# Optimization experiments

Hardware: AMD Instinct MI355X
Metric: run time of the kernel (lower is better)

## Reference

```python
import jax, jax.numpy as jnp
import numpy as np
import math

B, S, D_MODEL = 2, 2048, 1024
H = 16
DK = D_MODEL // H          # 64, down-proj per-stream dim
NOPE, ROPE = 128, 64
D_HEAD = NOPE + ROPE       # 192 = d_latent // H
D_LATENT = H * D_HEAD      # 3072
ROT_DIM = 2 * ((ROPE // 2) // 2)  # rotary dim actually rotated = qk_rope_dim//2 = 32
EPS = 1e-6


def _rmsnorm(x, w):
    out = x * jax.lax.rsqrt(jnp.mean(x * x, axis=-1, keepdims=True) + EPS)
    return out * w


def _apply_rope(x):
    # x: [b, h, s, d]; rotate first ROT_DIM channels, interleaved pairing
    s = x.shape[-2]
    inv_freq = 1.0 / (10000.0 ** (jnp.arange(0, ROT_DIM, 2, dtype=jnp.float32) / ROT_DIM))
    freqs = jnp.arange(s, dtype=jnp.float32)[:, None] * inv_freq[None, :]  # [s, ROT_DIM//2]
    freqs = jnp.repeat(freqs, 2, axis=-1)  # [s, ROT_DIM], (f0,f0,f1,f1,...)
    cos, sin = jnp.cos(freqs), jnp.sin(freqs)
    xl, xr = x[..., :ROT_DIM], x[..., ROT_DIM:]
    x1, x2 = xl[..., 0::2], xl[..., 1::2]
    rot = jnp.stack([-x2, x1], axis=-1).reshape(xl.shape)
    xl = xl * cos + rot * sin
    return jnp.concatenate([xl, xr], axis=-1)


def setup_inputs() -> dict:
    key = jax.random.key(0)
    ks = jax.random.split(key, 5)
    sc = 0.02
    x = jax.random.normal(ks[0], (B, S, D_MODEL), jnp.float32)
    mask = jnp.broadcast_to(jnp.tril(jnp.ones((S, S), jnp.int32)), (B, S, S))
    w_down = jax.random.normal(ks[1], (D_MODEL, 3 * DK), jnp.float32) * sc
    rms_w = jnp.ones((3 * DK,), jnp.float32)
    w_up = jax.random.normal(ks[2], (3 * DK, 3 * D_LATENT), jnp.float32) * sc
    w_o = jax.random.normal(ks[3], (D_LATENT, D_MODEL), jnp.float32) * sc
    return {"x": x, "mask": mask, "w_down": w_down, "rms_w": rms_w, "w_up": w_up, "w_o": w_o}


def reference(x, mask, w_down, rms_w, w_up, w_o):
    h = x @ w_down                        # [b, s, 3*dk]
    h = _rmsnorm(h, rms_w)
    qkv = h @ w_up                        # [b, s, 3*d_latent]
    q, k, v = jnp.split(qkv, 3, axis=-1)  # each [b, s, d_latent]

    def to_heads(t):
        # einops '(d h)': d outer, h inner
        return t.reshape(B, S, D_HEAD, H).transpose(0, 3, 1, 2)  # [b, h, s, d]

    q, k, v = to_heads(q), to_heads(k), to_heads(v)
    q_nope, q_rope = q[..., :NOPE], q[..., NOPE:]
    k_nope, k_rope = k[..., :NOPE], k[..., NOPE:]
    q_rope = _apply_rope(q_rope)
    k_rope = _apply_rope(k_rope)

    scores = (jnp.einsum('bhid,bhjd->bhij', q_nope, k_nope)
              + jnp.einsum('bhid,bhjd->bhij', q_rope, k_rope))
    scores = scores / math.sqrt(NOPE + ROPE)
    scores = jnp.where(mask[:, None] == 0, -1e9, scores)
    attn = jax.nn.softmax(scores, axis=-1)

    out = jnp.einsum('bhij,bhjd->bhid', attn, v)        # [b, h, s, d]
    out = out.transpose(0, 2, 1, 3).reshape(B, S, D_LATENT)  # 'b h s d -> b s (h d)'
    return out @ w_o
```

## Files before the change

### kernel.cpp

```cpp
#include <hip/hip_runtime.h>
#include <stdint.h>
#include <stddef.h>


typedef __bf16 bf16x8 __attribute__((ext_vector_type(8)));
typedef float  f32x4  __attribute__((ext_vector_type(4)));

#define MFMA16x16(a,b,c) __builtin_amdgcn_mfma_f32_16x16x32_bf16((a),(b),(c),0,0,0)

__device__ __forceinline__ uint16_t f2bf(float f){
  union { float f; uint32_t u; } v; v.f = f;
  uint32_t u = v.u + 0x7fffu + ((v.u >> 16) & 1u);
  return (uint16_t)(u >> 16);
}
__device__ __forceinline__ bf16x8 load_frag(const uint16_t* p){
  uint4 u = *reinterpret_cast<const uint4*>(p);
  return __builtin_bit_cast(bf16x8, u);
}
__device__ __forceinline__ f32x4 fzero(){
  f32x4 z = {0.f, 0.f, 0.f, 0.f};
  return z;
}
__device__ __forceinline__ uint32_t pack2(float a, float b){
  return (uint32_t)f2bf(a) | ((uint32_t)f2bf(b) << 16);
}
__device__ __forceinline__ void gl2lds16(const uint16_t* g, uint16_t* l){
  __builtin_amdgcn_global_load_lds(
      (const __attribute__((address_space(1))) uint32_t*)g,
      (__attribute__((address_space(3))) uint32_t*)l,
      16, 0, 0);
}

__global__ __launch_bounds__(256) void k_transpose_cvt(const float* __restrict__ in,
                                                       uint16_t* __restrict__ out,
                                                       int R, int C){
  __shared__ float t[32][33];
  const int tc = blockIdx.x * 32;
  const int tr = blockIdx.y * 32;
  const int j = threadIdx.x & 31, i0 = threadIdx.x >> 5;
  for(int ii = 0; ii < 4; ++ii){
    int r = i0 + ii * 8;
    t[r][j] = in[(size_t)(tr + r) * C + tc + j];
  }
  __syncthreads();
  for(int ii = 0; ii < 4; ++ii){
    int c = i0 + ii * 8;
    out[(size_t)(tc + c) * R + tr + j] = f2bf(t[j][c]);
  }
}

__global__ __launch_bounds__(256) void k_down_mfma(const float* __restrict__ x,
                                                   const uint16_t* __restrict__ wdt,
                                                   const float* __restrict__ rms_w,
                                                   uint16_t* __restrict__ h_out){
  __shared__ __align__(16) uint16_t as[32 * 64];
  __shared__ float hsq[32];
  const int tid  = threadIdx.x;
  const int wave = tid >> 6, lane = tid & 63;
  const int ml = lane & 15, qd = lane >> 4;
  const int m0 = blockIdx.x * 32;
  const int n0w = wave * 48;
  if(tid < 32) hsq[tid] = 0.f;

  f32x4 acc[2][3];
#pragma unroll
  for(int mt = 0; mt < 2; ++mt)
#pragma unroll
    for(int nt = 0; nt < 3; ++nt) acc[mt][nt] = fzero();

  const int srow = tid >> 3, sc = tid & 7;
  for(int kt = 0; kt < 16; ++kt){
    const float* src = x + (size_t)(m0 + srow) * 1024 + kt * 64 + sc * 8;
    float4 a = *reinterpret_cast<const float4*>(src);
    float4 b = *reinterpret_cast<const float4*>(src + 4);
    uint4 pk;
    pk.x = pack2(a.x, a.y); pk.y = pack2(a.z, a.w);
    pk.z = pack2(b.x, b.y); pk.w = pack2(b.z, b.w);
    __syncthreads();
    *reinterpret_cast<uint4*>(as + srow * 64 + ((sc ^ (srow & 7)) * 8)) = pk;
    __syncthreads();
#pragma unroll
    for(int kk = 0; kk < 2; ++kk){
      bf16x8 af[2];
#pragma unroll
      for(int mt = 0; mt < 2; ++mt){
        int row = mt * 16 + ml;
        af[mt] = load_frag(as + row * 64 + (((kk * 4 + qd) ^ (row & 7)) * 8));
      }
#pragma unroll
      for(int nt = 0; nt < 3; ++nt){
        bf16x8 bfr = load_frag(wdt + (size_t)(n0w + nt * 16 + ml) * 1024 + kt * 64 + kk * 32 + qd * 8);
#pragma unroll
        for(int mt = 0; mt < 2; ++mt)
          acc[mt][nt] = MFMA16x16(af[mt], bfr, acc[mt][nt]);
      }
    }
  }
  __syncthreads();
#pragma unroll
  for(int mt = 0; mt < 2; ++mt)
#pragma unroll
    for(int r = 0; r < 4; ++r){
      float s = acc[mt][0][r]*acc[mt][0][r] + acc[mt][1][r]*acc[mt][1][r] + acc[mt][2][r]*acc[mt][2][r];
#pragma unroll
      for(int off = 1; off < 16; off <<= 1) s += __shfl_xor(s, off);
      if(ml == 0) atomicAdd(&hsq[mt * 16 + qd * 4 + r], s);
    }
  __syncthreads();
  float rw[3];
#pragma unroll
  for(int nt = 0; nt < 3; ++nt) rw[nt] = rms_w[n0w + nt * 16 + ml];
#pragma unroll
  for(int mt = 0; mt < 2; ++mt)
#pragma unroll
    for(int r = 0; r < 4; ++r){
      int row = mt * 16 + qd * 4 + r;
      float scl = rsqrtf(hsq[row] * (1.0f / 192.0f) + 1e-6f);
#pragma unroll
      for(int nt = 0; nt < 3; ++nt)
        h_out[(size_t)(m0 + row) * 192 + n0w + nt * 16 + ml] = f2bf(acc[mt][nt][r] * scl * rw[nt]);
    }
}

__global__ __launch_bounds__(256) void k_gemm_up(const uint16_t* __restrict__ hmat,
                                                 const uint16_t* __restrict__ wt,
                                                 uint16_t* __restrict__ q_t,
                                                 uint16_t* __restrict__ k_t,
                                                 uint16_t* __restrict__ v_t){
  __shared__ __align__(16) uint16_t rp[16 * 129 * 8];
  const int wave = threadIdx.x >> 6, lane = threadIdx.x & 63;
  const int ml = lane & 15, qd = lane >> 4;
  const int m0 = blockIdx.y * 32;
  const int bx = blockIdx.x;
  const int which = bx / 6;
  const int d0b = (bx % 6) * 32;
  const int n0w = bx * 512 + wave * 128;
  const int d0w = d0b + wave * 8;

  bf16x8 af[2][6];
#pragma unroll
  for(int mt = 0; mt < 2; ++mt)
#pragma unroll
    for(int kk = 0; kk < 6; ++kk)
      af[mt][kk] = load_frag(hmat + (size_t)(m0 + mt * 16 + ml) * 192 + kk * 32 + qd * 8);

  f32x4 acc[8][2];
#pragma unroll
  for(int nt = 0; nt < 8; ++nt){ acc[nt][0] = fzero(); acc[nt][1] = fzero(); }
#pragma unroll
  for(int nt = 0; nt < 8; ++nt){
#pragma unroll
    for(int kk = 0; kk < 6; ++kk){
      bf16x8 b = load_frag(wt + (size_t)(n0w + nt * 16 + ml) * 192 + kk * 32 + qd * 8);
      acc[nt][0] = MFMA16x16(af[0][kk], b, acc[nt][0]);
      acc[nt][1] = MFMA16x16(af[1][kk], b, acc[nt][1]);
    }
  }

  const int b   = m0 >> 11;
  const int s0  = m0 & 2047;
  const int kt2 = s0 >> 6;
  const int row0 = s0 & 63;
  uint4* rp4 = (uint4*)rp;

  if(which < 2){
    const float qs = which ? 1.0f : 0.07216878364870322f;
    const bool rope = (d0w >= 128) && (d0w < 160);
#pragma unroll
    for(int mt = 0; mt < 2; ++mt)
#pragma unroll
      for(int r = 0; r < 4; ++r){
        int t = mt * 16 + qd * 4 + r;
        int s = s0 + t;
        float v[8];
#pragma unroll
        for(int nt = 0; nt < 8; ++nt) v[nt] = acc[nt][mt][r] * qs;
        if(rope){
#pragma unroll
          for(int pi = 0; pi < 4; ++pi){
            int fi = (d0w + 2 * pi - 128) >> 1;
            float invf = __expf(-(float)fi * 0.5756462732485114f);
            float sn, cs;
            sincosf((float)s * invf, &sn, &cs);
            float e = v[2 * pi], o = v[2 * pi + 1];
            v[2 * pi]     = e * cs - o * sn;
            v[2 * pi + 1] = o * cs + e * sn;
          }
        }
        uint4 pk;
        pk.x = pack2(v[0], v[1]); pk.y = pack2(v[2], v[3]);
        pk.z = pack2(v[4], v[5]); pk.w = pack2(v[6], v[7]);
        rp4[ml * 129 + t * 4 + (wave ^ (t & 3))] = pk;
      }
  } else {
#pragma unroll
    for(int nt = 0; nt < 8; ++nt){
      int dl = wave * 8 + nt;
#pragma unroll
      for(int mt = 0; mt < 2; ++mt){
        int jc = mt * 2 + (qd >> 1);
        int slot = ml * 129 + dl * 4 + (jc ^ (dl & 3));
        uint2 pk;
        pk.x = pack2(acc[nt][mt][0], acc[nt][mt][1]);
        pk.y = pack2(acc[nt][mt][2], acc[nt][mt][3]);
        *(reinterpret_cast<uint2*>(rp + slot * 8) + (qd & 1)) = pk;
      }
    }
  }
  __syncthreads();

  if(which < 2){
    uint16_t* dst = which ? k_t : q_t;
    const int cb = d0b >> 3;
#pragma unroll
    for(int it = 0; it < 8; ++it){
      int h = wave * 4 + (it & 3), rhalf = it >> 2;
      int tloc = rhalf * 16 + (lane >> 2), p = lane & 3;
      int row = row0 + tloc;
      uint4 val = rp4[h * 129 + tloc * 4 + p];
      size_t off = ((size_t)(b * 16 + h) * 32 + kt2) * 12288
                 + (size_t)row * 192 + ((cb ^ (tloc & 4)) + p) * 8;
      *reinterpret_cast<uint4*>(dst + off) = val;
    }
  } else {
    const int cs0 = row0 >> 3;
#pragma unroll
    for(int it = 0; it < 8; ++it){
      int h = wave * 4 + (it & 3), dhalf = it >> 2;
      int dl = dhalf * 16 + (lane >> 2), p = lane & 3;
      uint4 val = rp4[h * 129 + dl * 4 + p];
      size_t off = ((size_t)(b * 16 + h) * 32 + kt2) * 12288
                 + (size_t)(d0b + dl) * 64 + ((cs0 ^ (dl & 4)) + p) * 8;
      *reinterpret_cast<uint4*>(v_t + off) = val;
    }
  }
}

__global__ __launch_bounds__(512, 4) void k_attn(const uint16_t* __restrict__ q_t,
                                                 const uint16_t* __restrict__ k_t,
                                                 const uint16_t* __restrict__ v_t,
                                                 uint16_t* __restrict__ attn_out){
  __shared__ __align__(16) uint16_t smem[30720];
  const int tid  = threadIdx.x;
  const int wave = tid >> 6;
  const int lane = tid & 63;
  const int ml   = lane & 15;
  const int qd   = lane >> 4;
  const int B    = blockIdx.x;
  const int bh   = B & 31;
  const int prr  = B >> 5;
  const int qb   = (prr < 8) ? (15 - prr) : (prr - 8);
  const int last = 4 * qb + 3;

  uint16_t* const kbuf0 = smem;
  uint16_t* const kbuf1 = smem + 6144;
  uint16_t* const vbuf0 = smem + 12288;
  uint16_t* const vbuf1 = smem + 18944;
  uint16_t* const psw   = smem + 25600 + wave * 640;

  const uint16_t* kbase = k_t + (size_t)bh * 393216;
  const uint16_t* vbase = v_t + (size_t)bh * 393216;
  const uint16_t* qbase = q_t + (size_t)bh * 393216 + (size_t)qb * 24576;
  const int hh = bh & 15, bb = bh >> 4;

  int voffE[3], voffO[3];
  {
    const int w3 = (wave & 3) * 3;
#pragma unroll
    for(int it = 0; it < 3; ++it){
      int seg = w3 + it;
      int rp_ = seg * 8 + (lane >> 3);
      int x   = (lane & 7) ^ (rp_ & 7);
      int d   = rp_ * 2 + (x >> 2);
      int c   = x & 3;
      voffE[it] = d * 64 + (((0 + c) ^ (d & 7)) * 8);
      voffO[it] = d * 64 + (((4 + c) ^ (d & 7)) * 8);
    }
  }
  const int vpoff = (ml >> 1) * 64 + ((((ml & 1) * 4 + qd) ^ (ml >> 1)) * 8);

  {
    const int s0 = wave * 6;
#pragma unroll
    for(int it = 0; it < 6; ++it){
      int seg = s0 + it;
      gl2lds16(qbase + seg * 512 + lane * 8, smem + seg * 512);
    }
  }
  __builtin_amdgcn_sched_barrier(0);
  asm volatile("s_waitcnt vmcnt(0)" ::: "memory");
  __builtin_amdgcn_sched_barrier(0);
  __builtin_amdgcn_s_barrier();

  bf16x8 qf[6];
  {
    int row = wave * 16 + ml;
#pragma unroll
    for(int kk = 0; kk < 6; ++kk)
      qf[kk] = load_frag(smem + row * 192 + (((kk * 4 + qd) ^ (row & 7)) * 8));
  }
  asm volatile("s_waitcnt lgkmcnt(0)" ::: "memory");
  __builtin_amdgcn_sched_barrier(0);
  __builtin_amdgcn_s_barrier();

  if(tid < 256) ((uint32_t*)(vbuf0 + 6144))[tid] = 0x3F803F80u;
  else          ((uint32_t*)(vbuf1 + 6144))[tid - 256] = 0x3F803F80u;

  auto stage = [&](int t, int sel){
    const int w3 = (wave & 3) * 3;
    if(wave < 4){
      const uint16_t* src = kbase + t * 6144 + w3 * 512 + lane * 8;
      uint16_t* dst = (sel ? kbuf1 : kbuf0) + w3 * 512;
      gl2lds16(src, dst);
      gl2lds16(src + 512, dst + 512);
      gl2lds16(src + 1024, dst + 1024);
    } else {
      const uint16_t* srcb = vbase + (size_t)(t >> 1) * 12288;
      uint16_t* dst = (sel ? vbuf1 : vbuf0) + w3 * 512;
      if(t & 1){
        gl2lds16(srcb + voffO[0], dst);
        gl2lds16(srcb + voffO[1], dst + 512);
        gl2lds16(srcb + voffO[2], dst + 1024);
      } else {
        gl2lds16(srcb + voffE[0], dst);
        gl2lds16(srcb + voffE[1], dst + 512);
        gl2lds16(srcb + voffE[2], dst + 1024);
      }
    }
  };

  stage(0, 0);

  f32x4 o[13];
#pragma unroll
  for(int i = 0; i < 13; ++i) o[i] = fzero();

  const int r0 = qb * 128 + wave * 16;
  int cur = 0;
  for(int kt = 0; kt <= last; ++kt){
    if(kt < last){
      stage(kt + 1, cur ^ 1);
      __builtin_amdgcn_sched_barrier(0);
      asm volatile("s_waitcnt vmcnt(3)" ::: "memory");
      __builtin_amdgcn_sched_barrier(0);
    } else {
      asm volatile("s_waitcnt vmcnt(0)" ::: "memory");
      __builtin_amdgcn_sched_barrier(0);
    }
    __builtin_amdgcn_s_barrier();

    if(kt * 32 <= r0 + 15){
      const uint16_t* kc = cur ? kbuf1 : kbuf0;
      const uint16_t* vc = cur ? vbuf1 : vbuf0;
      float p[2][4];
      __builtin_amdgcn_s_setprio(1);
#pragma unroll
      for(int nt = 0; nt < 2; ++nt){
        f32x4 a = fzero();
        int row = nt * 16 + ml;
#pragma unroll
        for(int kk = 0; kk < 6; ++kk){
          bf16x8 b = load_frag(kc + row * 192 + (((kk * 4 + qd) ^ (row & 7)) * 8));
          a = MFMA16x16(qf[kk], b, a);
        }
#pragma unroll
        for(int r = 0; r < 4; ++r) p[nt][r] = a[r];
      }
      __builtin_amdgcn_s_setprio(0);
      const bool diag = (kt * 32 + 31 > r0);
#pragma unroll
      for(int nt = 0; nt < 2; ++nt)
#pragma unroll
        for(int r = 0; r < 4; ++r){
          float v = p[nt][r];
          if(diag){
            int i = r0 + qd * 4 + r;
            int j = kt * 32 + nt * 16 + ml;
            if(j > i) v = -1e9f;
          }
          p[nt][r] = __expf(v);
        }
#pragma unroll
      for(int nt = 0; nt < 2; ++nt)
#pragma unroll
        for(int r = 0; r < 4; ++r)
          psw[(qd * 4 + r) * 40 + nt * 16 + ml] = f2bf(p[nt][r]);
      bf16x8 pa = load_frag(psw + ml * 40 + qd * 8);
      __builtin_amdgcn_s_setprio(1);
#pragma unroll
      for(int dt = 0; dt < 13; ++dt){
        bf16x8 vbf = load_frag(vc + vpoff + dt * 512);
        o[dt] = MFMA16x16(pa, vbf, o[dt]);
      }
      __builtin_amdgcn_s_setprio(0);
    }
    __builtin_amdgcn_s_barrier();
    cur ^= 1;
  }

#pragma unroll
  for(int r = 0; r < 4; ++r){
    int i = r0 + qd * 4 + r;
    float inv = 1.0f / o[12][r];
    size_t obase = ((size_t)bb * 2048 + i) * 3072 + hh * 192;
#pragma unroll
    for(int dt = 0; dt < 12; ++dt)
      attn_out[obase + dt * 16 + ml] = f2bf(o[dt][r] * inv);
  }
}

__global__ __launch_bounds__(256) void k_gemm_o_tile(const uint16_t* __restrict__ a,
                                                     const uint16_t* __restrict__ wt,
                                                     float* __restrict__ part){
  __shared__ __align__(16) uint16_t as[128 * 64];
  __shared__ __align__(16) uint16_t bs[128 * 64];
  const int wave = threadIdx.x >> 6, lane = threadIdx.x & 63;
  const int ml = lane & 15, qd = lane >> 4;
  const int m0 = blockIdx.y * 128, n0 = blockIdx.x * 128;
  const int kz = blockIdx.z;
  const int mo = (wave >> 1) * 64, no = (wave & 1) * 64;

  const int lrow = lane >> 3;
  const int gch  = (lane & 7) ^ (lrow & 7);
  const uint16_t* abase = a  + (size_t)(m0 + lrow) * 3072 + kz * 1536 + gch * 8;
  const uint16_t* bbase = wt + (size_t)(n0 + lrow) * 3072 + kz * 1536 + gch * 8;

  f32x4 acc[4][4];
#pragma unroll
  for(int mt = 0; mt < 4; ++mt)
#pragma unroll
    for(int nt = 0; nt < 4; ++nt) acc[mt][nt] = fzero();

  for(int kt = 0; kt < 24; ++kt){
    __syncthreads();
#pragma unroll
    for(int it = 0; it < 4; ++it){
      int seg = it * 4 + wave;
      gl2lds16(abase + (size_t)seg * 24576 + kt * 64, as + seg * 512);
      gl2lds16(bbase + (size_t)seg * 24576 + kt * 64, bs + seg * 512);
    }
    __syncthreads();
#pragma unroll
    for(int ks2 = 0; ks2 < 2; ++ks2){
      bf16x8 af[4], bfr[4];
#pragma unroll
      for(int mt = 0; mt < 4; ++mt){
        int row = mo + mt * 16 + ml;
        af[mt] = load_frag(as + row * 64 + (((ks2 * 4 + qd) ^ (row & 7)) * 8));
      }
#pragma unroll
      for(int nt = 0; nt < 4; ++nt){
        int row = no + nt * 16 + ml;
        bfr[nt] = load_frag(bs + row * 64 + (((ks2 * 4 + qd) ^ (row & 7)) * 8));
      }
#pragma unroll
      for(int mt = 0; mt < 4; ++mt)
#pragma unroll
        for(int nt = 0; nt < 4; ++nt)
          acc[mt][nt] = MFMA16x16(af[mt], bfr[nt], acc[mt][nt]);
    }
  }

  float* dst = part + (size_t)kz * 4096 * 1024;
#pragma unroll
  for(int mt = 0; mt < 4; ++mt)
#pragma unroll
    for(int nt = 0; nt < 4; ++nt)
#pragma unroll
      for(int r = 0; r < 4; ++r){
        int row = m0 + mo + mt * 16 + qd * 4 + r;
        int col = n0 + no + nt * 16 + ml;
        dst[(size_t)row * 1024 + col] = acc[mt][nt][r];
      }
}

__global__ __launch_bounds__(256) void k_addout(const float* __restrict__ part,
                                                float* __restrict__ out){
  int i = blockIdx.x * 256 + threadIdx.x;
  const float4* p0 = (const float4*)part;
  const float4* p1 = p0 + (size_t)1048576;
  float4 a = p0[i], b = p1[i];
  float4 c; c.x = a.x + b.x; c.y = a.y + b.y; c.z = a.z + b.z; c.w = a.w + b.w;
  ((float4*)out)[i] = c;
}


extern "C" void kernel_launch(void* const* d_in, const int* in_sizes, int n_in,
                              void* d_out, int out_size, void* d_ws, size_t ws_size,
                              hipStream_t stream) {
  (void)in_sizes; (void)n_in; (void)out_size; (void)ws_size;
  const float* x      = (const float*)d_in[0];
  const float* w_down = (const float*)d_in[2];
  const float* rms_w  = (const float*)d_in[3];
  const float* w_up   = (const float*)d_in[4];
  const float* w_o    = (const float*)d_in[5];
  float* out = (float*)d_out;

  char* ws = (char*)d_ws;
  uint16_t* h_bf   = (uint16_t*)(ws);
  uint16_t* w_up_t = (uint16_t*)(ws + 1572864);
  uint16_t* w_o_t  = (uint16_t*)(ws + 5111808);
  uint16_t* w_dn_t = (uint16_t*)(ws + 11403264);
  uint16_t* q_tb   = (uint16_t*)(ws + 11796480);
  uint16_t* k_tb   = (uint16_t*)(ws + 36962304);
  uint16_t* v_tb   = (uint16_t*)(ws + 62128128);
  uint16_t* attnO  = (uint16_t*)(ws + 87293952);
  float*    part   = (float*)(ws + 11796480);

  k_transpose_cvt<<<dim3(288, 6), 256, 0, stream>>>(w_up, w_up_t, 192, 9216);
  k_transpose_cvt<<<dim3(32, 96), 256, 0, stream>>>(w_o,  w_o_t,  3072, 1024);
  k_transpose_cvt<<<dim3(6, 32),  256, 0, stream>>>(w_down, w_dn_t, 1024, 192);
  k_down_mfma<<<128, 256, 0, stream>>>(x, w_dn_t, rms_w, h_bf);
  k_gemm_up<<<dim3(18, 128), 256, 0, stream>>>(h_bf, w_up_t, q_tb, k_tb, v_tb);
  k_attn<<<512, 512, 0, stream>>>(q_tb, k_tb, v_tb, attnO);
  k_gemm_o_tile<<<dim3(8, 32, 2), 256, 0, stream>>>(attnO, w_o_t, part);
  k_addout<<<4096, 256, 0, stream>>>(part, out);
}
```

Measured before the change: 348.5 us.

## Split attention keys across wave halves and pair causal query blocks per workgroup

Rebuilds the attention kernel around 64-row query blocks. Each workgroup handles two of them (31-p and p) so causal work is balanced across workgroups. Within a block, the 8 waves split into 4 query strips times 2 key halves, and the two halves' partial outputs are summed through shared memory. The aim is to even out the causal triangle's load imbalance and get more MFMA work per K/V tile. In exchange it drops K/V double buffering: each tile load is waited on fully before compute. It also adds a cross-wave reduction and lowers the launch-bounds occupancy hint from 4 to 2.

```diff
diff --git a/kernel.cpp b/kernel.cpp
--- a/kernel.cpp
+++ b/kernel.cpp
@@ -236,177 +236,159 @@
   }
 }
 
-__global__ __launch_bounds__(512, 4) void k_attn(const uint16_t* __restrict__ q_t,
+__global__ __launch_bounds__(512, 2) void k_attn(const uint16_t* __restrict__ q_t,
                                                  const uint16_t* __restrict__ k_t,
                                                  const uint16_t* __restrict__ v_t,
                                                  uint16_t* __restrict__ attn_out){
   __shared__ __align__(16) uint16_t smem[30720];
-  const int tid  = threadIdx.x;
-  const int wave = tid >> 6;
-  const int lane = tid & 63;
-  const int ml   = lane & 15;
-  const int qd   = lane >> 4;
-  const int B    = blockIdx.x;
-  const int bh   = B & 31;
-  const int prr  = B >> 5;
-  const int qb   = (prr < 8) ? (15 - prr) : (prr - 8);
-  const int last = 4 * qb + 3;
-
-  uint16_t* const kbuf0 = smem;
-  uint16_t* const kbuf1 = smem + 6144;
-  uint16_t* const vbuf0 = smem + 12288;
-  uint16_t* const vbuf1 = smem + 18944;
-  uint16_t* const psw   = smem + 25600 + wave * 640;
+  const int tid   = threadIdx.x;
+  const int wave  = tid >> 6;
+  const int lane  = tid & 63;
+  const int ml    = lane & 15;
+  const int qd    = lane >> 4;
+  const int strip = wave & 3;
+  const int khalf = wave >> 2;
+  const int B     = blockIdx.x;
+  const int bh    = B & 31;
+  const int p     = B >> 5;
+
+  uint16_t* const kb  = smem;
+  uint16_t* const vb  = smem + 12288;
+  uint16_t* const psw = smem + 25600 + wave * 640;
 
   const uint16_t* kbase = k_t + (size_t)bh * 393216;
   const uint16_t* vbase = v_t + (size_t)bh * 393216;
-  const uint16_t* qbase = q_t + (size_t)bh * 393216 + (size_t)qb * 24576;
+  const uint16_t* qbase = q_t + (size_t)bh * 393216;
   const int hh = bh & 15, bb = bh >> 4;
 
-  int voffE[3], voffO[3];
-  {
-    const int w3 = (wave & 3) * 3;
+  auto stageKV = [&](int kt){
+    const uint16_t* ksrc = kbase + (size_t)kt * 12288;
+    const uint16_t* vsrc = vbase + (size_t)kt * 12288;
 #pragma unroll
     for(int it = 0; it < 3; ++it){
-      int seg = w3 + it;
-      int rp_ = seg * 8 + (lane >> 3);
-      int x   = (lane & 7) ^ (rp_ & 7);
-      int d   = rp_ * 2 + (x >> 2);
-      int c   = x & 3;
-      voffE[it] = d * 64 + (((0 + c) ^ (d & 7)) * 8);
-      voffO[it] = d * 64 + (((4 + c) ^ (d & 7)) * 8);
-    }
-  }
-  const int vpoff = (ml >> 1) * 64 + ((((ml & 1) * 4 + qd) ^ (ml >> 1)) * 8);
-
-  {
-    const int s0 = wave * 6;
-#pragma unroll
-    for(int it = 0; it < 6; ++it){
-      int seg = s0 + it;
-      gl2lds16(qbase + seg * 512 + lane * 8, smem + seg * 512);
-    }
-  }
-  __builtin_amdgcn_sched_barrier(0);
-  asm volatile("s_waitcnt vmcnt(0)" ::: "memory");
-  __builtin_amdgcn_sched_barrier(0);
-  __builtin_amdgcn_s_barrier();
-
-  bf16x8 qf[6];
-  {
-    int row = wave * 16 + ml;
-#pragma unroll
-    for(int kk = 0; kk < 6; ++kk)
-      qf[kk] = load_frag(smem + row * 192 + (((kk * 4 + qd) ^ (row & 7)) * 8));
-  }
-  asm volatile("s_waitcnt lgkmcnt(0)" ::: "memory");
-  __builtin_amdgcn_sched_barrier(0);
-  __builtin_amdgcn_s_barrier();
-
-  if(tid < 256) ((uint32_t*)(vbuf0 + 6144))[tid] = 0x3F803F80u;
-  else          ((uint32_t*)(vbuf1 + 6144))[tid - 256] = 0x3F803F80u;
-
-  auto stage = [&](int t, int sel){
-    const int w3 = (wave & 3) * 3;
-    if(wave < 4){
-      const uint16_t* src = kbase + t * 6144 + w3 * 512 + lane * 8;
-      uint16_t* dst = (sel ? kbuf1 : kbuf0) + w3 * 512;
-      gl2lds16(src, dst);
-      gl2lds16(src + 512, dst + 512);
-      gl2lds16(src + 1024, dst + 1024);
-    } else {
-      const uint16_t* srcb = vbase + (size_t)(t >> 1) * 12288;
-      uint16_t* dst = (sel ? vbuf1 : vbuf0) + w3 * 512;
-      if(t & 1){
-        gl2lds16(srcb + voffO[0], dst);
-        gl2lds16(srcb + voffO[1], dst + 512);
-        gl2lds16(srcb + voffO[2], dst + 1024);
-      } else {
-        gl2lds16(srcb + voffE[0], dst);
-        gl2lds16(srcb + voffE[1], dst + 512);
-        gl2lds16(srcb + voffE[2], dst + 1024);
-      }
+      int seg = wave * 3 + it;
+      gl2lds16(ksrc + seg * 512 + lane * 8, kb + seg * 512);
+    }
+#pragma unroll
+    for(int it = 0; it < 3; ++it){
+      int seg = wave * 3 + it;
+      gl2lds16(vsrc + seg * 512 + lane * 8, vb + seg * 512);
     }
   };
 
-  stage(0, 0);
-
-  f32x4 o[13];
-#pragma unroll
-  for(int i = 0; i < 13; ++i) o[i] = fzero();
-
-  const int r0 = qb * 128 + wave * 16;
-  int cur = 0;
-  for(int kt = 0; kt <= last; ++kt){
-    if(kt < last){
-      stage(kt + 1, cur ^ 1);
+  auto run_qblock = [&](int qb){
+    {
+      const uint16_t* qtile = qbase + (size_t)qb * 12288;
+#pragma unroll
+      for(int it = 0; it < 3; ++it){
+        int seg = wave * 3 + it;
+        gl2lds16(qtile + seg * 512 + lane * 8, kb + seg * 512);
+      }
+    }
+    __builtin_amdgcn_sched_barrier(0);
+    asm volatile("s_waitcnt vmcnt(0)" ::: "memory");
+    __builtin_amdgcn_sched_barrier(0);
+    __builtin_amdgcn_s_barrier();
+
+    bf16x8 qf[6];
+    {
+      int row = strip * 16 + ml;
+#pragma unroll
+      for(int kk = 0; kk < 6; ++kk)
+        qf[kk] = load_frag(kb + row * 192 + (((kk * 4 + qd) ^ (row & 7)) * 8));
+    }
+    ((uint32_t*)vb)[6144 + tid] = 0x3F803F80u;
+    __syncthreads();
+
+    stageKV(0);
+
+    f32x4 o[13];
+#pragma unroll
+    for(int i = 0; i < 13; ++i) o[i] = fzero();
+
+    const int r0 = qb * 64 + strip * 16;
+    for(int kt = 0; kt <= qb; ++kt){
       __builtin_amdgcn_sched_barrier(0);
-      asm volatile("s_waitcnt vmcnt(3)" ::: "memory");
-      __builtin_amdgcn_sched_barrier(0);
-    } else {
       asm volatile("s_waitcnt vmcnt(0)" ::: "memory");
       __builtin_amdgcn_sched_barrier(0);
-    }
-    __builtin_amdgcn_s_barrier();
-
-    if(kt * 32 <= r0 + 15){
-      const uint16_t* kc = cur ? kbuf1 : kbuf0;
-      const uint16_t* vc = cur ? vbuf1 : vbuf0;
-      float p[2][4];
-      __builtin_amdgcn_s_setprio(1);
-#pragma unroll
-      for(int nt = 0; nt < 2; ++nt){
-        f32x4 a = fzero();
-        int row = nt * 16 + ml;
-#pragma unroll
-        for(int kk = 0; kk < 6; ++kk){
-          bf16x8 b = load_frag(kc + row * 192 + (((kk * 4 + qd) ^ (row & 7)) * 8));
-          a = MFMA16x16(qf[kk], b, a);
+      __builtin_amdgcn_s_barrier();
+
+      const int kl = kt * 64 + khalf * 32;
+      if(kl <= r0 + 15){
+        float pp[2][4];
+        __builtin_amdgcn_s_setprio(1);
+#pragma unroll
+        for(int nt = 0; nt < 2; ++nt){
+          f32x4 a = fzero();
+          int row = khalf * 32 + nt * 16 + ml;
+#pragma unroll
+          for(int kk = 0; kk < 6; ++kk){
+            bf16x8 bfr = load_frag(kb + row * 192 + (((kk * 4 + qd) ^ (row & 7)) * 8));
+            a = MFMA16x16(qf[kk], bfr, a);
+          }
+#pragma unroll
+          for(int r = 0; r < 4; ++r) pp[nt][r] = a[r];
         }
-#pragma unroll
-        for(int r = 0; r < 4; ++r) p[nt][r] = a[r];
-      }
-      __builtin_amdgcn_s_setprio(0);
-      const bool diag = (kt * 32 + 31 > r0);
-#pragma unroll
-      for(int nt = 0; nt < 2; ++nt)
-#pragma unroll
-        for(int r = 0; r < 4; ++r){
-          float v = p[nt][r];
-          if(diag){
-            int i = r0 + qd * 4 + r;
-            int j = kt * 32 + nt * 16 + ml;
-            if(j > i) v = -1e9f;
+        __builtin_amdgcn_s_setprio(0);
+        const bool diag = (kl + 31 > r0);
+#pragma unroll
+        for(int nt = 0; nt < 2; ++nt)
+#pragma unroll
+          for(int r = 0; r < 4; ++r){
+            float v = pp[nt][r];
+            if(diag){
+              int i = r0 + qd * 4 + r;
+              int j = kl + nt * 16 + ml;
+              if(j > i) v = -1e9f;
+            }
+            pp[nt][r] = __expf(v);
           }
-          p[nt][r] = __expf(v);
+#pragma unroll
+        for(int nt = 0; nt < 2; ++nt)
+#pragma unroll
+          for(int r = 0; r < 4; ++r)
+            psw[(qd * 4 + r) * 40 + nt * 16 + ml] = f2bf(pp[nt][r]);
+        bf16x8 pa = load_frag(psw + ml * 40 + qd * 8);
+        __builtin_amdgcn_s_setprio(1);
+#pragma unroll
+        for(int dt = 0; dt < 13; ++dt){
+          int row = dt * 16 + ml;
+          int cv = (khalf * 4 + qd) ^ (row & 7);
+          bf16x8 vbf = load_frag(vb + row * 64 + cv * 8);
+          o[dt] = MFMA16x16(pa, vbf, o[dt]);
         }
-#pragma unroll
-      for(int nt = 0; nt < 2; ++nt)
-#pragma unroll
-        for(int r = 0; r < 4; ++r)
-          psw[(qd * 4 + r) * 40 + nt * 16 + ml] = f2bf(p[nt][r]);
-      bf16x8 pa = load_frag(psw + ml * 40 + qd * 8);
-      __builtin_amdgcn_s_setprio(1);
-#pragma unroll
-      for(int dt = 0; dt < 13; ++dt){
-        bf16x8 vbf = load_frag(vc + vpoff + dt * 512);
-        o[dt] = MFMA16x16(pa, vbf, o[dt]);
-      }
-      __builtin_amdgcn_s_setprio(0);
-    }
-    __builtin_amdgcn_s_barrier();
-    cur ^= 1;
-  }
-
-#pragma unroll
-  for(int r = 0; r < 4; ++r){
-    int i = r0 + qd * 4 + r;
-    float inv = 1.0f / o[12][r];
-    size_t obase = ((size_t)bb * 2048 + i) * 3072 + hh * 192;
-#pragma unroll
-    for(int dt = 0; dt < 12; ++dt)
-      attn_out[obase + dt * 16 + ml] = f2bf(o[dt][r] * inv);
-  }
+        __builtin_amdgcn_s_setprio(0);
+      }
+      __builtin_amdgcn_s_barrier();
+      if(kt < qb) stageKV(kt + 1);
+    }
+
+    f32x4* red4 = (f32x4*)smem;
+    if(khalf == 1){
+#pragma unroll
+      for(int dt = 0; dt < 13; ++dt)
+        red4[strip * 832 + lane * 13 + dt] = o[dt];
+    }
+    __syncthreads();
+    if(khalf == 0){
+#pragma unroll
+      for(int dt = 0; dt < 13; ++dt)
+        o[dt] += red4[strip * 832 + lane * 13 + dt];
+#pragma unroll
+      for(int r = 0; r < 4; ++r){
+        int i = r0 + qd * 4 + r;
+        float inv = 1.0f / o[12][r];
+        size_t obase = ((size_t)bb * 2048 + i) * 3072 + hh * 192;
+#pragma unroll
+        for(int dt = 0; dt < 12; ++dt)
+          attn_out[obase + dt * 16 + ml] = f2bf(o[dt][r] * inv);
+      }
+    }
+    __syncthreads();
+  };
+
+  run_qblock(31 - p);
+  run_qblock(p);
 }
 
 __global__ __launch_bounds__(256) void k_gemm_o_tile(const uint16_t* __restrict__ a,
```

New measurement: 365.8 us. 5.0% more time.
